# Kernel tuning notes

Hardware: AMD Instinct MI355X
Metric: run time of the kernel (lower is better)

## Reference

```python
import jax, jax.numpy as jnp
import numpy as np

B, S, D, H = 2, 2048, 1024, 16
HD = D // H  # head_dim = 64


def setup_inputs() -> dict:
    key = jax.random.key(0)
    k1, k2, k3, k4, k5 = jax.random.split(key, 5)
    x = jax.random.normal(k1, (B, S, D), dtype=jnp.float32)
    # causal additive mask [S, S]: 0 on/below diagonal, -1e9 above
    mask = jnp.where(jnp.tril(jnp.ones((S, S), dtype=bool)), 0.0, -1e9).astype(jnp.float32)
    scale = 1.0 / np.sqrt(D)
    W_qkv = jax.random.normal(k2, (D, 3 * D), dtype=jnp.float32) * scale
    b_qkv = jax.random.normal(k3, (3 * D,), dtype=jnp.float32) * 0.01
    W_o = jax.random.normal(k4, (D, D), dtype=jnp.float32) * scale
    b_o = jax.random.normal(k5, (D,), dtype=jnp.float32) * 0.01
    return {"x": x, "mask": mask, "W_qkv": W_qkv, "b_qkv": b_qkv, "W_o": W_o, "b_o": b_o}


def reference(x, mask, W_qkv, b_qkv, W_o, b_o):
    b, s, d = x.shape
    qkv = x @ W_qkv + b_qkv                         # [B,S,3D]
    qkv = qkv.reshape(b, s, H, 3 * HD).transpose(0, 2, 1, 3)  # [B,H,S,3*HD]
    q, k, v = jnp.split(qkv, 3, axis=-1)            # each [B,H,S,HD]
    scores = jnp.einsum('bhqd,bhkd->bhqk', q, k) / np.sqrt(HD)  # [B,H,S,S]
    scores = scores + mask                           # broadcast [S,S] additive mask
    attn = jax.nn.softmax(scores, axis=-1)
    vals = jnp.einsum('bhqk,bhkd->bhqd', attn, v)    # [B,H,S,HD]
    vals = vals.transpose(0, 2, 1, 3).reshape(b, s, d)
    return vals @ W_o + b_o
```

## Files before the change

### kernel.cpp

```cpp
#include <hip/hip_runtime.h>

#define NB 2
#define NS 2048
#define ND 1024
#define NH 16
#define NHD 64
#define QLD (3 * ND)
#define PADP 72
#define PADV 68

typedef unsigned short u16;
typedef __attribute__((ext_vector_type(8))) short short8;
typedef __attribute__((ext_vector_type(4))) short short4v;
typedef __attribute__((ext_vector_type(4))) float f32x4;

__device__ __forceinline__ u16 f2b(float f) {
    unsigned int x = __float_as_uint(f);
    return (u16)((x + 0x7fffu + ((x >> 16) & 1u)) >> 16);
}

__global__ __launch_bounds__(256) void convert_bf16(
    const float* __restrict__ src, u16* __restrict__ dst, int n)
{
    const int i = (blockIdx.x * 256 + threadIdx.x) * 8;
    if (i >= n) return;
    float4 a = *(const float4*)(src + i);
    float4 b = *(const float4*)(src + i + 4);
    *(ushort4*)(dst + i)     = make_ushort4(f2b(a.x), f2b(a.y), f2b(a.z), f2b(a.w));
    *(ushort4*)(dst + i + 4) = make_ushort4(f2b(b.x), f2b(b.y), f2b(b.z), f2b(b.w));
}

__global__ __launch_bounds__(256) void transpose_bf16(
    const float* __restrict__ W, u16* __restrict__ WT, int K, int N)
{
    __shared__ u16 Ts[64 * 72];
    const int t = threadIdx.x;
    const int k0 = blockIdx.y << 6, n0 = blockIdx.x << 6;
    const int r = t >> 4, c = (t & 15) << 2;
    #pragma unroll
    for (int rr = 0; rr < 64; rr += 16) {
        float4 v = *(const float4*)&W[(size_t)(k0 + r + rr) * N + n0 + c];
        Ts[(c + 0) * 72 + r + rr] = f2b(v.x);
        Ts[(c + 1) * 72 + r + rr] = f2b(v.y);
        Ts[(c + 2) * 72 + r + rr] = f2b(v.z);
        Ts[(c + 3) * 72 + r + rr] = f2b(v.w);
    }
    __syncthreads();
    const int n = t >> 2, cc = (t & 3) << 4;
    uint4 a = *(const uint4*)&Ts[n * 72 + cc];
    uint4 b = *(const uint4*)&Ts[n * 72 + cc + 8];
    *(uint4*)&WT[(size_t)(n0 + n) * K + k0 + cc]     = a;
    *(uint4*)&WT[(size_t)(n0 + n) * K + k0 + cc + 8] = b;
}

template <bool STORE_BF16>
__global__ __launch_bounds__(256) void gemm_mfma(
    const u16* __restrict__ A, const u16* __restrict__ BT,
    const float* __restrict__ bias,
    void* __restrict__ C, int M, int N, int K)
{
    __shared__ u16 As[128 * 32];
    __shared__ u16 Bs[128 * 32];

    const int tid = threadIdx.x;
    const int wave = tid >> 6, lane = tid & 63;
    const int col = lane & 15, quad = lane >> 4;
    const int wm = wave >> 1, wn = wave & 1;
    const int row0 = blockIdx.y << 7, col0 = blockIdx.x << 7;

    f32x4 acc[4][4] = {};

    const u16* asrc[2];
    const u16* bsrc[2];
    u16* adst[2];
    u16* bdst[2];
    #pragma unroll
    for (int is = 0; is < 2; ++is) {
        const int J = is * 256 + wave * 64 + lane;
        const int m = J >> 2;
        const int q = (J & 3) ^ ((m >> 1) & 3);
        asrc[is] = A  + (size_t)(row0 + m) * K + q * 8;
        bsrc[is] = BT + (size_t)(col0 + m) * K + q * 8;
        adst[is] = &As[(size_t)(is * 256 + wave * 64) * 8];
        bdst[is] = &Bs[(size_t)(is * 256 + wave * 64) * 8];
    }

    for (int kk = 0; kk < K; kk += 32) {
        __syncthreads();
        #pragma unroll
        for (int is = 0; is < 2; ++is) {
            __builtin_amdgcn_global_load_lds(
                (const __attribute__((address_space(1))) unsigned int*)(asrc[is] + kk),
                (__attribute__((address_space(3))) unsigned int*)adst[is], 16, 0, 0);
            __builtin_amdgcn_global_load_lds(
                (const __attribute__((address_space(1))) unsigned int*)(bsrc[is] + kk),
                (__attribute__((address_space(3))) unsigned int*)bdst[is], 16, 0, 0);
        }
        __syncthreads();

        short8 af[4], bf[4];
        #pragma unroll
        for (int i = 0; i < 4; ++i) {
            const int m = wm * 64 + i * 16 + col;
            af[i] = *(const short8*)&As[(m * 4 + (quad ^ ((m >> 1) & 3))) * 8];
        }
        #pragma unroll
        for (int j = 0; j < 4; ++j) {
            const int n = wn * 64 + j * 16 + col;
            bf[j] = *(const short8*)&Bs[(n * 4 + (quad ^ ((n >> 1) & 3))) * 8];
        }
        #pragma unroll
        for (int i = 0; i < 4; ++i)
            #pragma unroll
            for (int j = 0; j < 4; ++j)
                acc[i][j] = __builtin_amdgcn_mfma_f32_16x16x32_bf16(
                    af[i], bf[j], acc[i][j], 0, 0, 0);
    }

    #pragma unroll
    for (int j = 0; j < 4; ++j) {
        const int gc = col0 + wn * 64 + j * 16 + col;
        const float bj = bias[gc];
        #pragma unroll
        for (int i = 0; i < 4; ++i) {
            const int gr = row0 + wm * 64 + i * 16 + quad * 4;
            #pragma unroll
            for (int r = 0; r < 4; ++r) {
                const float v = acc[i][j][r] + bj;
                if (STORE_BF16)
                    ((u16*)C)[(size_t)(gr + r) * N + gc] = f2b(v);
                else
                    ((float*)C)[(size_t)(gr + r) * N + gc] = v;
            }
        }
    }
}

__global__ __launch_bounds__(256) void attn_kernel(
    const u16* __restrict__ qkv, u16* __restrict__ vals)
{
    __shared__ u16 Ks[2][64 * 64];
    __shared__ u16 Vt[2][64 * PADV];
    __shared__ u16 Ps[64 * PADP];

    const int tid = threadIdx.x;
    const int wave = tid >> 6, lane = tid & 63;
    const int col = lane & 15, quad = lane >> 4;
    const int qtA = blockIdx.x;
    const int qtB = 31 - qtA;
    const int bh = blockIdx.y;
    const int b = bh >> 4, h = bh & 15;
    const size_t base = (size_t)b * NS * QLD + (size_t)h * (3 * NHD);
    const int q0 = wave * 16;

    int Jrow[2], Jcol[2];
    #pragma unroll
    for (int is = 0; is < 2; ++is) {
        const int J = is * 256 + wave * 64 + lane;
        Jrow[is] = J >> 3;
        Jcol[is] = ((J & 7) ^ (Jrow[is] & 7)) << 3;
    }

    auto stage_tile = [&](int buf, int srow, int coloff) {
        #pragma unroll
        for (int is = 0; is < 2; ++is) {
            __builtin_amdgcn_global_load_lds(
                (const __attribute__((address_space(1))) unsigned int*)
                    (qkv + base + (size_t)(srow + Jrow[is]) * QLD + coloff + Jcol[is]),
                (__attribute__((address_space(3))) unsigned int*)
                    &Ks[buf][(size_t)(is * 256 + wave * 64) * 8], 16, 0, 0);
        }
    };
    auto read_frag = [&](int buf, int row, int half) -> short8 {
        const int blk = row * 8 + ((quad + (half << 2)) ^ (row & 7));
        return *(const short8*)&Ks[buf][blk << 3];
    };

    const int vtx = tid & 15, vty = tid >> 4;
    const int vk0 = vty << 2, vd0 = vtx << 2;
    auto load_vregs = [&](int kt, ushort4* vr) {
        const u16* vsrc = qkv + base + (size_t)(kt * 64 + vk0) * QLD + 2 * NHD + vd0;
        vr[0] = *(const ushort4*)(vsrc);
        vr[1] = *(const ushort4*)(vsrc + QLD);
        vr[2] = *(const ushort4*)(vsrc + 2 * QLD);
        vr[3] = *(const ushort4*)(vsrc + 3 * QLD);
    };
    auto write_vt = [&](int buf, const ushort4* vr) {
        *(ushort4*)&Vt[buf][(vd0 + 0) * PADV + vk0] =
            make_ushort4(vr[0].x, vr[1].x, vr[2].x, vr[3].x);
        *(ushort4*)&Vt[buf][(vd0 + 1) * PADV + vk0] =
            make_ushort4(vr[0].y, vr[1].y, vr[2].y, vr[3].y);
        *(ushort4*)&Vt[buf][(vd0 + 2) * PADV + vk0] =
            make_ushort4(vr[0].z, vr[1].z, vr[2].z, vr[3].z);
        *(ushort4*)&Vt[buf][(vd0 + 3) * PADV + vk0] =
            make_ushort4(vr[0].w, vr[1].w, vr[2].w, vr[3].w);
    };

    stage_tile(0, qtA * 64, 0);
    __syncthreads();
    short8 aqA0 = read_frag(0, q0 + col, 0);
    short8 aqA1 = read_frag(0, q0 + col, 1);
    __syncthreads();
    stage_tile(0, qtB * 64, 0);
    __syncthreads();
    short8 aqB0 = read_frag(0, q0 + col, 0);
    short8 aqB1 = read_frag(0, q0 + col, 1);
    __syncthreads();

    f32x4 accA[4] = {}, accB[4] = {};
    float mA[4], lA[4], mB[4], lB[4];
    #pragma unroll
    for (int r = 0; r < 4; ++r) { mA[r] = mB[r] = -1e30f; lA[r] = lB[r] = 0.f; }

    auto process = [&](const short8& a0, const short8& a1,
                       short8 (*kb)[2], short8 (*vb)[2],
                       f32x4* accO, float* mrow, float* lrow, bool diag) {
        f32x4 s[4] = {};
        #pragma unroll
        for (int kg = 0; kg < 4; ++kg) {
            s[kg] = __builtin_amdgcn_mfma_f32_16x16x32_bf16(a0, kb[kg][0], s[kg], 0, 0, 0);
            s[kg] = __builtin_amdgcn_mfma_f32_16x16x32_bf16(a1, kb[kg][1], s[kg], 0, 0, 0);
        }
        #pragma unroll
        for (int kg = 0; kg < 4; ++kg)
            #pragma unroll
            for (int r = 0; r < 4; ++r) {
                float v = s[kg][r] * 0.125f;
                if (diag && (kg * 16 + col > q0 + quad * 4 + r)) v = -1e30f;
                s[kg][r] = v;
            }
        float alpha[4];
        #pragma unroll
        for (int r = 0; r < 4; ++r) {
            float mx = fmaxf(fmaxf(s[0][r], s[1][r]), fmaxf(s[2][r], s[3][r]));
            mx = fmaxf(mx, __shfl_xor(mx, 1, 64));
            mx = fmaxf(mx, __shfl_xor(mx, 2, 64));
            mx = fmaxf(mx, __shfl_xor(mx, 4, 64));
            mx = fmaxf(mx, __shfl_xor(mx, 8, 64));
            float mn = fmaxf(mrow[r], mx);
            alpha[r] = __expf(mrow[r] - mn);
            mrow[r] = mn;
        }
        #pragma unroll
        for (int r = 0; r < 4; ++r) {
            float ps = 0.f;
            #pragma unroll
            for (int kg = 0; kg < 4; ++kg) {
                float p = __expf(s[kg][r] - mrow[r]);
                ps += p;
                Ps[(q0 + quad * 4 + r) * PADP + kg * 16 + col] = f2b(p);
            }
            ps += __shfl_xor(ps, 1, 64);
            ps += __shfl_xor(ps, 2, 64);
            ps += __shfl_xor(ps, 4, 64);
            ps += __shfl_xor(ps, 8, 64);
            lrow[r] = lrow[r] * alpha[r] + ps;
            #pragma unroll
            for (int dg = 0; dg < 4; ++dg) accO[dg][r] *= alpha[r];
        }
        short8 ap0 = *(const short8*)&Ps[(q0 + col) * PADP + quad * 8];
        short8 ap1 = *(const short8*)&Ps[(q0 + col) * PADP + 32 + quad * 8];
        #pragma unroll
        for (int dg = 0; dg < 4; ++dg) {
            accO[dg] = __builtin_amdgcn_mfma_f32_16x16x32_bf16(ap0, vb[dg][0], accO[dg], 0, 0, 0);
            accO[dg] = __builtin_amdgcn_mfma_f32_16x16x32_bf16(ap1, vb[dg][1], accO[dg], 0, 0, 0);
        }
    };

    ushort4 vcur[4], vnxt[4];
    stage_tile(0, 0, NHD);
    load_vregs(0, vcur);

    for (int kt = 0; kt <= qtB; ++kt) {
        const int cur = kt & 1, nxt = cur ^ 1;
        __syncthreads();
        write_vt(cur, vcur);
        __syncthreads();

        if (kt < qtB) {
            stage_tile(nxt, (kt + 1) * 64, NHD);
            load_vregs(kt + 1, vnxt);
        }

        short8 kb[4][2], vb[4][2];
        #pragma unroll
        for (int kg = 0; kg < 4; ++kg) {
            kb[kg][0] = read_frag(cur, kg * 16 + col, 0);
            kb[kg][1] = read_frag(cur, kg * 16 + col, 1);
        }
        #pragma unroll
        for (int dg = 0; dg < 4; ++dg) {
            const int n = dg * 16 + col;
            short4v lo0 = *(const short4v*)&Vt[cur][n * PADV + quad * 8];
            short4v hi0 = *(const short4v*)&Vt[cur][n * PADV + quad * 8 + 4];
            short4v lo1 = *(const short4v*)&Vt[cur][n * PADV + 32 + quad * 8];
            short4v hi1 = *(const short4v*)&Vt[cur][n * PADV + 32 + quad * 8 + 4];
            vb[dg][0] = __builtin_shufflevector(lo0, hi0, 0, 1, 2, 3, 4, 5, 6, 7);
            vb[dg][1] = __builtin_shufflevector(lo1, hi1, 0, 1, 2, 3, 4, 5, 6, 7);
        }

        process(aqB0, aqB1, kb, vb, accB, mB, lB, kt == qtB);
        if (kt <= qtA)
            process(aqA0, aqA1, kb, vb, accA, mA, lA, kt == qtA);

        #pragma unroll
        for (int i = 0; i < 4; ++i) vcur[i] = vnxt[i];
    }

    #pragma unroll
    for (int r = 0; r < 4; ++r) {
        const float invA = 1.f / lA[r];
        const float invB = 1.f / lB[r];
        const size_t rowA = ((size_t)b * NS + qtA * 64 + q0 + quad * 4 + r) * ND + h * NHD;
        const size_t rowB = ((size_t)b * NS + qtB * 64 + q0 + quad * 4 + r) * ND + h * NHD;
        #pragma unroll
        for (int dg = 0; dg < 4; ++dg) {
            vals[rowA + dg * 16 + col] = f2b(accA[dg][r] * invA);
            vals[rowB + dg * 16 + col] = f2b(accB[dg][r] * invB);
        }
    }
}

extern "C" void kernel_launch(void* const* d_in, const int* in_sizes, int n_in,
                              void* d_out, int out_size, void* d_ws, size_t ws_size,
                              hipStream_t stream)
{
    const float* x    = (const float*)d_in[0];
    const float* Wqkv = (const float*)d_in[2];
    const float* bqkv = (const float*)d_in[3];
    const float* Wo   = (const float*)d_in[4];
    const float* bo   = (const float*)d_in[5];
    float* out = (float*)d_out;

    u16* x_bf   = (u16*)d_ws;
    u16* WqkvT  = x_bf   + (size_t)4096 * 1024;
    u16* WoT    = WqkvT  + (size_t)3072 * 1024;
    u16* qkv    = WoT    + (size_t)1024 * 1024;
    u16* vals   = qkv    + (size_t)4096 * 3072;

    const int M = NB * NS;

    convert_bf16<<<dim3(M * ND / (256 * 8)), dim3(256), 0, stream>>>(
        x, x_bf, M * ND);
    transpose_bf16<<<dim3(QLD / 64, ND / 64), dim3(256), 0, stream>>>(
        Wqkv, WqkvT, ND, QLD);
    transpose_bf16<<<dim3(ND / 64, ND / 64), dim3(256), 0, stream>>>(
        Wo, WoT, ND, ND);

    gemm_mfma<true><<<dim3(QLD / 128, M / 128), dim3(256), 0, stream>>>(
        x_bf, WqkvT, bqkv, qkv, M, QLD, ND);
    attn_kernel<<<dim3(16, NB * NH), dim3(256), 0, stream>>>(qkv, vals);
    gemm_mfma<false><<<dim3(ND / 128, M / 128), dim3(256), 0, stream>>>(
        vals, WoT, bo, out, M, ND, ND);
}
```

Baseline: 238.1 us.

## Swap MFMA operands so each lane owns one query row in attention

Computes S^T and O^T by swapping the A/B MFMA operands, so each lane holds a single query row's values across its accumulator registers. Row max and sum now need two cross-lane shuffles instead of four per row, with one scalar m/l per lane. P and output writes become 4-element vector stores. The Q tiles for both query blocks are also staged together with one fewer sync pair. The cost is a different LDS write pattern for P, which could change bank conflicts.

```diff
diff --git a/kernel.cpp b/kernel.cpp
--- a/kernel.cpp
+++ b/kernel.cpp
@@ -152,6 +152,7 @@
     const int b = bh >> 4, h = bh & 15;
     const size_t base = (size_t)b * NS * QLD + (size_t)h * (3 * NHD);
     const int q0 = wave * 16;
+    const int qloc = q0 + col;
 
     int Jrow[2], Jcol[2];
     #pragma unroll
@@ -197,73 +198,67 @@
     };
 
     stage_tile(0, qtA * 64, 0);
+    stage_tile(1, qtB * 64, 0);
     __syncthreads();
-    short8 aqA0 = read_frag(0, q0 + col, 0);
-    short8 aqA1 = read_frag(0, q0 + col, 1);
+    short8 bqA0 = read_frag(0, qloc, 0), bqA1 = read_frag(0, qloc, 1);
+    short8 bqB0 = read_frag(1, qloc, 0), bqB1 = read_frag(1, qloc, 1);
     __syncthreads();
-    stage_tile(0, qtB * 64, 0);
-    __syncthreads();
-    short8 aqB0 = read_frag(0, q0 + col, 0);
-    short8 aqB1 = read_frag(0, q0 + col, 1);
-    __syncthreads();
 
     f32x4 accA[4] = {}, accB[4] = {};
-    float mA[4], lA[4], mB[4], lB[4];
-    #pragma unroll
-    for (int r = 0; r < 4; ++r) { mA[r] = mB[r] = -1e30f; lA[r] = lB[r] = 0.f; }
-
-    auto process = [&](const short8& a0, const short8& a1,
+    float mA = -1e30f, lA = 0.f, mB = -1e30f, lB = 0.f;
+
+    auto process = [&](const short8& b0, const short8& b1,
                        short8 (*kb)[2], short8 (*vb)[2],
-                       f32x4* accO, float* mrow, float* lrow, bool diag) {
+                       f32x4* accO, float& m, float& l, bool diag) {
         f32x4 s[4] = {};
         #pragma unroll
         for (int kg = 0; kg < 4; ++kg) {
-            s[kg] = __builtin_amdgcn_mfma_f32_16x16x32_bf16(a0, kb[kg][0], s[kg], 0, 0, 0);
-            s[kg] = __builtin_amdgcn_mfma_f32_16x16x32_bf16(a1, kb[kg][1], s[kg], 0, 0, 0);
+            s[kg] = __builtin_amdgcn_mfma_f32_16x16x32_bf16(kb[kg][0], b0, s[kg], 0, 0, 0);
+            s[kg] = __builtin_amdgcn_mfma_f32_16x16x32_bf16(kb[kg][1], b1, s[kg], 0, 0, 0);
         }
         #pragma unroll
         for (int kg = 0; kg < 4; ++kg)
             #pragma unroll
             for (int r = 0; r < 4; ++r) {
                 float v = s[kg][r] * 0.125f;
-                if (diag && (kg * 16 + col > q0 + quad * 4 + r)) v = -1e30f;
+                if (diag && (kg * 16 + quad * 4 + r > qloc)) v = -1e30f;
                 s[kg][r] = v;
             }
-        float alpha[4];
-        #pragma unroll
-        for (int r = 0; r < 4; ++r) {
-            float mx = fmaxf(fmaxf(s[0][r], s[1][r]), fmaxf(s[2][r], s[3][r]));
-            mx = fmaxf(mx, __shfl_xor(mx, 1, 64));
-            mx = fmaxf(mx, __shfl_xor(mx, 2, 64));
-            mx = fmaxf(mx, __shfl_xor(mx, 4, 64));
-            mx = fmaxf(mx, __shfl_xor(mx, 8, 64));
-            float mn = fmaxf(mrow[r], mx);
-            alpha[r] = __expf(mrow[r] - mn);
-            mrow[r] = mn;
-        }
-        #pragma unroll
-        for (int r = 0; r < 4; ++r) {
-            float ps = 0.f;
+        float mx = -1e30f;
+        #pragma unroll
+        for (int kg = 0; kg < 4; ++kg)
+            mx = fmaxf(mx, fmaxf(fmaxf(s[kg][0], s[kg][1]), fmaxf(s[kg][2], s[kg][3])));
+        mx = fmaxf(mx, __shfl_xor(mx, 16, 64));
+        mx = fmaxf(mx, __shfl_xor(mx, 32, 64));
+        const float mn = fmaxf(m, mx);
+        const float alpha = __expf(m - mn);
+        m = mn;
+
+        float ps = 0.f;
+        #pragma unroll
+        for (int kg = 0; kg < 4; ++kg) {
+            float p0 = __expf(s[kg][0] - mn);
+            float p1 = __expf(s[kg][1] - mn);
+            float p2 = __expf(s[kg][2] - mn);
+            float p3 = __expf(s[kg][3] - mn);
+            ps += (p0 + p1) + (p2 + p3);
+            *(ushort4*)&Ps[qloc * PADP + kg * 16 + quad * 4] =
+                make_ushort4(f2b(p0), f2b(p1), f2b(p2), f2b(p3));
+        }
+        ps += __shfl_xor(ps, 16, 64);
+        ps += __shfl_xor(ps, 32, 64);
+        l = l * alpha + ps;
+        #pragma unroll
+        for (int dg = 0; dg < 4; ++dg)
             #pragma unroll
-            for (int kg = 0; kg < 4; ++kg) {
-                float p = __expf(s[kg][r] - mrow[r]);
-                ps += p;
-                Ps[(q0 + quad * 4 + r) * PADP + kg * 16 + col] = f2b(p);
-            }
-            ps += __shfl_xor(ps, 1, 64);
-            ps += __shfl_xor(ps, 2, 64);
-            ps += __shfl_xor(ps, 4, 64);
-            ps += __shfl_xor(ps, 8, 64);
-            lrow[r] = lrow[r] * alpha[r] + ps;
-            #pragma unroll
-            for (int dg = 0; dg < 4; ++dg) accO[dg][r] *= alpha[r];
-        }
-        short8 ap0 = *(const short8*)&Ps[(q0 + col) * PADP + quad * 8];
-        short8 ap1 = *(const short8*)&Ps[(q0 + col) * PADP + 32 + quad * 8];
+            for (int r = 0; r < 4; ++r) accO[dg][r] *= alpha;
+
+        short8 pb0 = *(const short8*)&Ps[qloc * PADP + quad * 8];
+        short8 pb1 = *(const short8*)&Ps[qloc * PADP + 32 + quad * 8];
         #pragma unroll
         for (int dg = 0; dg < 4; ++dg) {
-            accO[dg] = __builtin_amdgcn_mfma_f32_16x16x32_bf16(ap0, vb[dg][0], accO[dg], 0, 0, 0);
-            accO[dg] = __builtin_amdgcn_mfma_f32_16x16x32_bf16(ap1, vb[dg][1], accO[dg], 0, 0, 0);
+            accO[dg] = __builtin_amdgcn_mfma_f32_16x16x32_bf16(vb[dg][0], pb0, accO[dg], 0, 0, 0);
+            accO[dg] = __builtin_amdgcn_mfma_f32_16x16x32_bf16(vb[dg][1], pb1, accO[dg], 0, 0, 0);
         }
     };
 
@@ -276,7 +271,6 @@
         __syncthreads();
         write_vt(cur, vcur);
         __syncthreads();
-
         if (kt < qtB) {
             stage_tile(nxt, (kt + 1) * 64, NHD);
             load_vregs(kt + 1, vnxt);
@@ -299,24 +293,38 @@
             vb[dg][1] = __builtin_shufflevector(lo1, hi1, 0, 1, 2, 3, 4, 5, 6, 7);
         }
 
-        process(aqB0, aqB1, kb, vb, accB, mB, lB, kt == qtB);
+        process(bqB0, bqB1, kb, vb, accB, mB, lB, kt == qtB);
         if (kt <= qtA)
-            process(aqA0, aqA1, kb, vb, accA, mA, lA, kt == qtA);
+            process(bqA0, bqA1, kb, vb, accA, mA, lA, kt == qtA);
 
         #pragma unroll
         for (int i = 0; i < 4; ++i) vcur[i] = vnxt[i];
     }
 
-    #pragma unroll
-    for (int r = 0; r < 4; ++r) {
-        const float invA = 1.f / lA[r];
-        const float invB = 1.f / lB[r];
-        const size_t rowA = ((size_t)b * NS + qtA * 64 + q0 + quad * 4 + r) * ND + h * NHD;
-        const size_t rowB = ((size_t)b * NS + qtB * 64 + q0 + quad * 4 + r) * ND + h * NHD;
+    {
+        const float inv = 1.f / lA;
+        const size_t rowoff = ((size_t)b * NS + qtA * 64 + qloc) * ND + h * NHD;
         #pragma unroll
         for (int dg = 0; dg < 4; ++dg) {
-            vals[rowA + dg * 16 + col] = f2b(accA[dg][r] * invA);
-            vals[rowB + dg * 16 + col] = f2b(accB[dg][r] * invB);
+            ushort4 o;
+            o.x = f2b(accA[dg][0] * inv);
+            o.y = f2b(accA[dg][1] * inv);
+            o.z = f2b(accA[dg][2] * inv);
+            o.w = f2b(accA[dg][3] * inv);
+            *(ushort4*)(vals + rowoff + dg * 16 + quad * 4) = o;
+        }
+    }
+    {
+        const float inv = 1.f / lB;
+        const size_t rowoff = ((size_t)b * NS + qtB * 64 + qloc) * ND + h * NHD;
+        #pragma unroll
+        for (int dg = 0; dg < 4; ++dg) {
+            ushort4 o;
+            o.x = f2b(accB[dg][0] * inv);
+            o.y = f2b(accB[dg][1] * inv);
+            o.z = f2b(accB[dg][2] * inv);
+            o.w = f2b(accB[dg][3] * inv);
+            *(ushort4*)(vals + rowoff + dg * 16 + quad * 4) = o;
         }
     }
 }
```

Result: faster. 219.9 us (-7.6%).
